# Kernel optimization log

Measured on AMD Instinct MI355X. Metric: run time of the kernel, lower is better.

## Reference

```python
import jax, jax.numpy as jnp
import numpy as np

SIGMA = 1.0  # init kwarg sigma

def _rbf_kernel(A):
    # K[i,j] = exp(-0.5 * ||a_i - a_j||^2 / sigma^2)
    sq = jnp.sum(A * A, axis=1)                      # [n]
    d2 = sq[:, None] + sq[None, :] - 2.0 * (A @ A.T)  # [n, n]
    return jnp.exp(-0.5 * d2 / (SIGMA ** 2))

def _double_center(K):
    # C K C with C = I - 11^T/n, done in O(n^2) via mean subtraction
    row = K.mean(axis=1, keepdims=True)
    col = K.mean(axis=0, keepdims=True)
    tot = K.mean()
    return K - row - col + tot

def setup_inputs() -> dict:
    key = jax.random.key(0)
    kx, ky = jax.random.split(key)
    X = jax.random.normal(kx, (4096, 512), dtype=jnp.float32)
    Y = jax.random.normal(ky, (4096, 512), dtype=jnp.float32)
    return {"X": X, "Y": Y}

def reference(X, Y):
    n = X.shape[0]
    KXc = _double_center(_rbf_kernel(X))
    KYc = _double_center(_rbf_kernel(Y))
    # trace(KX C KY C) = sum(center(KX) * center(KY)) since K symmetric, C idempotent
    hsic = jnp.sum(KXc * KYc) / ((n - 1) ** 2)
    return hsic
```

## Files before the change

kernel.cpp:

```cpp
#include <hip/hip_runtime.h>
#include <hip/hip_bf16.h>

namespace {

constexpr int N = 4096;
constexpr int D = 512;
constexpr int BM = 128;
constexpr int BK = 64;
constexpr int KITERS = D / BK;
constexpr int NB = N / BM;
constexpr int NBLK = NB * (NB + 1) / 2;
constexpr int TILEB = BM * BK;
constexpr int PANELB = BM * D;

constexpr size_t OFF_XB  = 0;
constexpr size_t OFF_YB  = (size_t)N * D;
constexpr size_t OFF_SQX = OFF_YB + (size_t)N * D;
constexpr size_t OFF_SQY = OFF_SQX + (size_t)N * 4;
constexpr size_t OFF_SX  = OFF_SQY + (size_t)N * 4;
constexpr size_t OFF_SY  = OFF_SX + (size_t)N * 4;
constexpr size_t OFF_T1  = OFF_SY + (size_t)N * 4;
constexpr size_t WS_NEED = OFF_T1 + 4;


constexpr float D2_SKIP = 240.f;

typedef __attribute__((ext_vector_type(4))) float floatx4;
typedef __attribute__((ext_vector_type(2))) long longx2;

__device__ inline void stage16(const void* g, void* l) {
  __builtin_amdgcn_global_load_lds(
      (const __attribute__((address_space(1))) unsigned int*)g,
      (__attribute__((address_space(3))) unsigned int*)l, 16, 0, 0);
}

__global__ void prep_kernel(const float* __restrict__ X, const float* __restrict__ Y,
                            unsigned char* __restrict__ Xf8, unsigned char* __restrict__ Yf8,
                            float* __restrict__ sqX, float* __restrict__ sqY,
                            float* __restrict__ sX, float* __restrict__ sY,
                            float* __restrict__ T1) {
  const int wave = threadIdx.x >> 6, lane = threadIdx.x & 63;
  const int row = blockIdx.x * 4 + wave;
  const int m = blockIdx.y;
  const float* __restrict__ src = m ? Y : X;
  unsigned char* __restrict__ dst = m ? Yf8 : Xf8;
  float* __restrict__ dsq = m ? sqY : sqX;

  if (threadIdx.x < 4) {
    float* z = m ? sY : sX;
    z[blockIdx.x * 4 + threadIdx.x] = 0.f;
  }
  if (blockIdx.x == 0 && m == 0 && threadIdx.x == 0) *T1 = 0.f;

  const float4* s4 = (const float4*)(src + (size_t)row * D);
  float4 v0 = s4[lane * 2];
  float4 v1 = s4[lane * 2 + 1];
  float acc = v0.x * v0.x + v0.y * v0.y + v0.z * v0.z + v0.w * v0.w
            + v1.x * v1.x + v1.y * v1.y + v1.z * v1.z + v1.w * v1.w;

  unsigned int w0 = 0, w1 = 0;
  w0 = __builtin_amdgcn_cvt_pk_fp8_f32(v0.x, v0.y, w0, false);
  w0 = __builtin_amdgcn_cvt_pk_fp8_f32(v0.z, v0.w, w0, true);
  w1 = __builtin_amdgcn_cvt_pk_fp8_f32(v1.x, v1.y, w1, false);
  w1 = __builtin_amdgcn_cvt_pk_fp8_f32(v1.z, v1.w, w1, true);
  const unsigned long long pk =
      (unsigned long long)w0 | ((unsigned long long)w1 << 32);

  const int p    = row >> 7;
  const int half = (row >> 6) & 1;
  const int nib  = (row >> 4) & 3;
  const int cl   = row & 15;
  const int ks   = lane >> 3;
  const int pass = (lane >> 2) & 1;
  const int quad = lane & 3;
  const size_t off = (size_t)p * PANELB + (size_t)ks * TILEB +
                     half * 4096 + nib * 1024 + quad * 256 + cl * 16 + pass * 8;
  *(unsigned long long*)(dst + off) = pk;

#pragma unroll
  for (int mm = 32; mm >= 1; mm >>= 1) acc += __shfl_xor(acc, mm, 64);
  if (lane == 0) dsq[row] = acc;
}

__launch_bounds__(256, 3)
__global__ void hsic_main(const unsigned char* __restrict__ Xf8,
                          const unsigned char* __restrict__ Yf8,
                          const float* __restrict__ sqX, const float* __restrict__ sqY,
                          float* __restrict__ sX, float* __restrict__ sY,
                          float* __restrict__ T1) {
  __shared__ __align__(16) unsigned char smem[2][2 * TILEB];

  const int b = blockIdx.x;
  int idx = (b & 7) * (NBLK / 8) + (b >> 3);

  const float nf = (float)NB + 0.5f;
  int bI = (int)(nf - sqrtf(nf * nf - 2.0f * (float)idx));
  if (bI < 0) bI = 0;
  if (bI >= NB) bI = NB - 1;
  while (bI * NB - bI * (bI - 1) / 2 > idx) --bI;
  while ((bI + 1) * NB - (bI + 1) * bI / 2 <= idx) ++bI;
  const int bJ = bI + (idx - (bI * NB - bI * (bI - 1) / 2));
  const bool offdiag = (bI != bJ);

  const int tid = threadIdx.x;
  const int lane = tid & 63, wave = tid >> 6;
  const int wm = wave >> 1, wn = wave & 1;
  const int quad = lane >> 4, cl = lane & 15;

  const unsigned char* gAx = Xf8 + (size_t)bI * PANELB;
  const unsigned char* gBx = Xf8 + (size_t)bJ * PANELB;
  const unsigned char* gAy = Yf8 + (size_t)bI * PANELB;
  const unsigned char* gBy = Yf8 + (size_t)bJ * PANELB;

  floatx4 accX[4][4];
  floatx4 accY[4][4];
#pragma unroll
  for (int i = 0; i < 4; ++i)
#pragma unroll
    for (int j = 0; j < 4; ++j) {
      accX[i][j] = (floatx4){0.f, 0.f, 0.f, 0.f};
      accY[i][j] = (floatx4){0.f, 0.f, 0.f, 0.f};
    }

  auto stage_all = [&](int iter, int buf) {
    const unsigned char* gA = (iter < KITERS) ? gAx : gAy;
    const unsigned char* gB = (iter < KITERS) ? gBx : gBy;
    const size_t ks0 = (size_t)(iter & (KITERS - 1)) * TILEB;
#pragma unroll
    for (int h = 0; h < 2; ++h) {
      const int c = tid + h * 256;
      const size_t goff = ks0 + (size_t)c * 16;
      stage16(gA + goff, &smem[buf][0 * TILEB + c * 16]);
      if (offdiag) stage16(gB + goff, &smem[buf][1 * TILEB + c * 16]);
    }
  };

  auto compute_tile = [&](const unsigned char* A, const unsigned char* B,
                          floatx4 (&acc)[4][4]) {
    longx2 bf[4];
#pragma unroll
    for (int ni = 0; ni < 4; ++ni)
      bf[ni] = *(const longx2*)&B[wn * 4096 + ni * 1024 + (lane << 4)];
#pragma unroll
    for (int mi = 0; mi < 4; ++mi) {
      const longx2 af = *(const longx2*)&A[wm * 4096 + mi * 1024 + (lane << 4)];
#pragma unroll
      for (int ni = 0; ni < 4; ++ni) {
        acc[mi][ni] = __builtin_amdgcn_mfma_f32_16x16x32_fp8_fp8(af[0], bf[ni][0], acc[mi][ni], 0, 0, 0);
        acc[mi][ni] = __builtin_amdgcn_mfma_f32_16x16x32_fp8_fp8(af[1], bf[ni][1], acc[mi][ni], 0, 0, 0);
      }
    }
  };

  stage_all(0, 0);

  for (int iter = 0; iter < 2 * KITERS; ++iter) {
    const int buf = iter & 1;
    __syncthreads();
    if (iter + 1 < 2 * KITERS) stage_all(iter + 1, buf ^ 1);

    const unsigned char* A = &smem[buf][0];
    const unsigned char* B = offdiag ? &smem[buf][TILEB] : &smem[buf][0];
    if (iter < KITERS) compute_tile(A, B, accX);
    else               compute_tile(A, B, accY);
  }

  const int Ib = bI * BM + wm * 64;
  const int Jb = bJ * BM + wn * 64;
  float t1l = 0.f;
  float rx[4][4], ry[4][4];
  float cx[4], cy[4];
#pragma unroll
  for (int mi = 0; mi < 4; ++mi)
#pragma unroll
    for (int r = 0; r < 4; ++r) { rx[mi][r] = 0.f; ry[mi][r] = 0.f; }
#pragma unroll
  for (int ni = 0; ni < 4; ++ni) { cx[ni] = 0.f; cy[ni] = 0.f; }

  bool wave_any = false;

#pragma unroll
  for (int mi = 0; mi < 4; ++mi) {
    const int ig0 = Ib + mi * 16 + quad * 4;
    float sxi[4], syi[4];
#pragma unroll
    for (int r = 0; r < 4; ++r) { sxi[r] = sqX[ig0 + r]; syi[r] = sqY[ig0 + r]; }
#pragma unroll
    for (int ni = 0; ni < 4; ++ni) {
      const int jg = Jb + ni * 16 + cl;
      const float sxj = sqX[jg];
      const float syj = sqY[jg];
      float d2x[4], d2y[4];
      bool lflag = false;
#pragma unroll
      for (int r = 0; r < 4; ++r) {
        const int ig = ig0 + r;
        d2x[r] = sxi[r] + sxj - 2.f * accX[mi][ni][r];
        d2y[r] = syi[r] + syj - 2.f * accY[mi][ni][r];
        lflag |= (d2x[r] < D2_SKIP) | (d2y[r] < D2_SKIP) | (ig == jg);
      }
      if (__any(lflag)) {
        wave_any = true;
#pragma unroll
        for (int r = 0; r < 4; ++r) {
          const int ig = ig0 + r;
          float kx, ky;
          if (ig == jg) {
            kx = 1.f; ky = 1.f;
          } else {
            kx = __expf(-0.5f * d2x[r]);
            ky = __expf(-0.5f * d2y[r]);
          }
          t1l += kx * ky;
          rx[mi][r] += kx;
          ry[mi][r] += ky;
          cx[ni] += kx;
          cy[ni] += ky;
        }
      }
    }
  }

  if (wave_any) {
#pragma unroll
    for (int mi = 0; mi < 4; ++mi)
#pragma unroll
      for (int r = 0; r < 4; ++r) {
        float vx = rx[mi][r], vy = ry[mi][r];
#pragma unroll
        for (int mm = 1; mm < 16; mm <<= 1) {
          vx += __shfl_xor(vx, mm, 16);
          vy += __shfl_xor(vy, mm, 16);
        }
        rx[mi][r] = vx; ry[mi][r] = vy;
      }
    if (cl == 0) {
#pragma unroll
      for (int mi = 0; mi < 4; ++mi)
#pragma unroll
        for (int r = 0; r < 4; ++r) {
          const int row = Ib + mi * 16 + quad * 4 + r;
          atomicAdd(&sX[row], rx[mi][r]);
          atomicAdd(&sY[row], ry[mi][r]);
        }
    }

    if (offdiag) {
#pragma unroll
      for (int ni = 0; ni < 4; ++ni) {
        float vx = cx[ni], vy = cy[ni];
        vx += __shfl_xor(vx, 16, 64); vy += __shfl_xor(vy, 16, 64);
        vx += __shfl_xor(vx, 32, 64); vy += __shfl_xor(vy, 32, 64);
        if (quad == 0) {
          const int col = Jb + ni * 16 + cl;
          atomicAdd(&sX[col], vx);
          atomicAdd(&sY[col], vy);
        }
      }
    }

    t1l *= offdiag ? 2.f : 1.f;
#pragma unroll
    for (int mm = 1; mm < 64; mm <<= 1) t1l += __shfl_xor(t1l, mm, 64);
  }
  __shared__ float tred[4];
  if (lane == 0) tred[wave] = t1l;
  __syncthreads();
  if (tid == 0) {
    const float t = tred[0] + tred[1] + tred[2] + tred[3];
    if (t != 0.f) atomicAdd(T1, t);
  }
}

__global__ void final_kernel(const float* __restrict__ sX, const float* __restrict__ sY,
                             const float* __restrict__ T1, float* __restrict__ out) {
  const int tid = threadIdx.x;
  float dp = 0.f, sa = 0.f, sb = 0.f;
  for (int i = tid; i < N; i += 256) {
    float a = sX[i], b = sY[i];
    dp += a * b; sa += a; sb += b;
  }
#pragma unroll
  for (int mm = 1; mm < 64; mm <<= 1) {
    dp += __shfl_xor(dp, mm, 64);
    sa += __shfl_xor(sa, mm, 64);
    sb += __shfl_xor(sb, mm, 64);
  }
  __shared__ float r0[4], r1[4], r2[4];
  if ((tid & 63) == 0) { int w = tid >> 6; r0[w] = dp; r1[w] = sa; r2[w] = sb; }
  __syncthreads();
  if (tid == 0) {
    dp = r0[0] + r0[1] + r0[2] + r0[3];
    sa = r1[0] + r1[1] + r1[2] + r1[3];
    sb = r2[0] + r2[1] + r2[2] + r2[3];
    const float n = (float)N;
    const float total = T1[0] - (2.f / n) * dp + (sa * sb) / (n * n);
    out[0] = total / ((n - 1.f) * (n - 1.f));
  }
}

}

extern "C" void kernel_launch(void* const* d_in, const int* in_sizes, int n_in,
                              void* d_out, int out_size, void* d_ws, size_t ws_size,
                              hipStream_t stream) {
  const float* X = (const float*)d_in[0];
  const float* Y = (const float*)d_in[1];
  char* ws = (char*)d_ws;
  if (ws_size < WS_NEED) return;

  unsigned char* Xf8 = (unsigned char*)(ws + OFF_XB);
  unsigned char* Yf8 = (unsigned char*)(ws + OFF_YB);
  float* sqX = (float*)(ws + OFF_SQX);
  float* sqY = (float*)(ws + OFF_SQY);
  float* sX  = (float*)(ws + OFF_SX);
  float* sY  = (float*)(ws + OFF_SY);
  float* T1  = (float*)(ws + OFF_T1);
  float* out = (float*)d_out;

  prep_kernel<<<dim3(N / 4, 2), 256, 0, stream>>>(X, Y, Xf8, Yf8, sqX, sqY, sX, sY, T1);
  hsic_main<<<NBLK, 256, 0, stream>>>(Xf8, Yf8, sqX, sqY, sX, sY, T1);
  final_kernel<<<1, 256, 0, stream>>>(sX, sY, T1, out);
}
```

Measured before the change: 97.22 us.

## Share one accumulator set across X and Y Gram passes, keeping X kernel as packed bf16

The main kernel now uses a single 4x4 block of MFMA accumulators instead of separate X and Y sets. The X-side RBF epilogue runs inside the k-loop right after the last X iteration: it computes the exp values, does the row and column atomics, packs the X kernel values into bf16 pairs and zeroes the accumulators for the Y pass. The Y epilogue then unpacks those values to form the cross term, with a per-tile mask marking which X sub-tiles were computed. This is meant to cut accumulator register pressure and raise occupancy, at the cost of bf16 rounding of the X kernel values in the HSIC sum.

Result: no change. 96.92 us (-0.3%).

```diff
diff --git a/kernel.cpp b/kernel.cpp
--- a/kernel.cpp
+++ b/kernel.cpp
@@ -32,6 +32,10 @@
   __builtin_amdgcn_global_load_lds(
       (const __attribute__((address_space(1))) unsigned int*)g,
       (__attribute__((address_space(3))) unsigned int*)l, 16, 0, 0);
+}
+
+__device__ inline unsigned short bf16bits(float f) {
+  return __builtin_bit_cast(unsigned short, __float2bfloat16(f));
 }
 
 __global__ void prep_kernel(const float* __restrict__ X, const float* __restrict__ Y,
@@ -112,15 +116,11 @@
   const unsigned char* gAy = Yf8 + (size_t)bI * PANELB;
   const unsigned char* gBy = Yf8 + (size_t)bJ * PANELB;
 
-  floatx4 accX[4][4];
-  floatx4 accY[4][4];
+  floatx4 acc[4][4];
 #pragma unroll
   for (int i = 0; i < 4; ++i)
 #pragma unroll
-    for (int j = 0; j < 4; ++j) {
-      accX[i][j] = (floatx4){0.f, 0.f, 0.f, 0.f};
-      accY[i][j] = (floatx4){0.f, 0.f, 0.f, 0.f};
-    }
+    for (int j = 0; j < 4; ++j) acc[i][j] = (floatx4){0.f, 0.f, 0.f, 0.f};
 
   auto stage_all = [&](int iter, int buf) {
     const unsigned char* gA = (iter < KITERS) ? gAx : gAy;
@@ -135,22 +135,12 @@
     }
   };
 
-  auto compute_tile = [&](const unsigned char* A, const unsigned char* B,
-                          floatx4 (&acc)[4][4]) {
-    longx2 bf[4];
-#pragma unroll
-    for (int ni = 0; ni < 4; ++ni)
-      bf[ni] = *(const longx2*)&B[wn * 4096 + ni * 1024 + (lane << 4)];
-#pragma unroll
-    for (int mi = 0; mi < 4; ++mi) {
-      const longx2 af = *(const longx2*)&A[wm * 4096 + mi * 1024 + (lane << 4)];
-#pragma unroll
-      for (int ni = 0; ni < 4; ++ni) {
-        acc[mi][ni] = __builtin_amdgcn_mfma_f32_16x16x32_fp8_fp8(af[0], bf[ni][0], acc[mi][ni], 0, 0, 0);
-        acc[mi][ni] = __builtin_amdgcn_mfma_f32_16x16x32_fp8_fp8(af[1], bf[ni][1], acc[mi][ni], 0, 0, 0);
-      }
-    }
-  };
+  const int Ib = bI * BM + wm * 64;
+  const int Jb = bJ * BM + wn * 64;
+
+  unsigned int kxp[4][4][2];
+  unsigned int fmask = 0;
+  float t1l = 0.f;
 
   stage_all(0, 0);
 
@@ -161,104 +151,177 @@
 
     const unsigned char* A = &smem[buf][0];
     const unsigned char* B = offdiag ? &smem[buf][TILEB] : &smem[buf][0];
-    if (iter < KITERS) compute_tile(A, B, accX);
-    else               compute_tile(A, B, accY);
-  }
-
-  const int Ib = bI * BM + wm * 64;
-  const int Jb = bJ * BM + wn * 64;
-  float t1l = 0.f;
-  float rx[4][4], ry[4][4];
-  float cx[4], cy[4];
-#pragma unroll
-  for (int mi = 0; mi < 4; ++mi)
-#pragma unroll
-    for (int r = 0; r < 4; ++r) { rx[mi][r] = 0.f; ry[mi][r] = 0.f; }
-#pragma unroll
-  for (int ni = 0; ni < 4; ++ni) { cx[ni] = 0.f; cy[ni] = 0.f; }
-
-  bool wave_any = false;
-
-#pragma unroll
-  for (int mi = 0; mi < 4; ++mi) {
-    const int ig0 = Ib + mi * 16 + quad * 4;
-    float sxi[4], syi[4];
-#pragma unroll
-    for (int r = 0; r < 4; ++r) { sxi[r] = sqX[ig0 + r]; syi[r] = sqY[ig0 + r]; }
-#pragma unroll
-    for (int ni = 0; ni < 4; ++ni) {
-      const int jg = Jb + ni * 16 + cl;
-      const float sxj = sqX[jg];
-      const float syj = sqY[jg];
-      float d2x[4], d2y[4];
-      bool lflag = false;
-#pragma unroll
-      for (int r = 0; r < 4; ++r) {
-        const int ig = ig0 + r;
-        d2x[r] = sxi[r] + sxj - 2.f * accX[mi][ni][r];
-        d2y[r] = syi[r] + syj - 2.f * accY[mi][ni][r];
-        lflag |= (d2x[r] < D2_SKIP) | (d2y[r] < D2_SKIP) | (ig == jg);
-      }
-      if (__any(lflag)) {
-        wave_any = true;
+
+    longx2 bf[4];
+#pragma unroll
+    for (int ni = 0; ni < 4; ++ni)
+      bf[ni] = *(const longx2*)&B[wn * 4096 + ni * 1024 + (lane << 4)];
+#pragma unroll
+    for (int mi = 0; mi < 4; ++mi) {
+      const longx2 af = *(const longx2*)&A[wm * 4096 + mi * 1024 + (lane << 4)];
+#pragma unroll
+      for (int ni = 0; ni < 4; ++ni) {
+        acc[mi][ni] = __builtin_amdgcn_mfma_f32_16x16x32_fp8_fp8(af[0], bf[ni][0], acc[mi][ni], 0, 0, 0);
+        acc[mi][ni] = __builtin_amdgcn_mfma_f32_16x16x32_fp8_fp8(af[1], bf[ni][1], acc[mi][ni], 0, 0, 0);
+      }
+    }
+
+    if (iter == KITERS - 1) {
+      float rx[4][4];
+      float cx[4];
+#pragma unroll
+      for (int mi = 0; mi < 4; ++mi)
+#pragma unroll
+        for (int r = 0; r < 4; ++r) rx[mi][r] = 0.f;
+#pragma unroll
+      for (int ni = 0; ni < 4; ++ni) cx[ni] = 0.f;
+
+#pragma unroll
+      for (int mi = 0; mi < 4; ++mi) {
+        const int ig0 = Ib + mi * 16 + quad * 4;
+        float sxi[4];
+#pragma unroll
+        for (int r = 0; r < 4; ++r) sxi[r] = sqX[ig0 + r];
+#pragma unroll
+        for (int ni = 0; ni < 4; ++ni) {
+          const int jg = Jb + ni * 16 + cl;
+          const float sxj = sqX[jg];
+          float d2x[4];
+          bool lflag = false;
+#pragma unroll
+          for (int r = 0; r < 4; ++r) {
+            const int ig = ig0 + r;
+            d2x[r] = sxi[r] + sxj - 2.f * acc[mi][ni][r];
+            lflag |= (d2x[r] < D2_SKIP) | (ig == jg);
+          }
+          float kxv[4] = {0.f, 0.f, 0.f, 0.f};
+          if (__any(lflag)) {
+            fmask |= (1u << (mi * 4 + ni));
+#pragma unroll
+            for (int r = 0; r < 4; ++r) {
+              const int ig = ig0 + r;
+              kxv[r] = (ig == jg) ? 1.f : __expf(-0.5f * d2x[r]);
+              rx[mi][r] += kxv[r];
+              cx[ni] += kxv[r];
+            }
+          }
+          kxp[mi][ni][0] = (unsigned)bf16bits(kxv[0]) | ((unsigned)bf16bits(kxv[1]) << 16);
+          kxp[mi][ni][1] = (unsigned)bf16bits(kxv[2]) | ((unsigned)bf16bits(kxv[3]) << 16);
+          acc[mi][ni] = (floatx4){0.f, 0.f, 0.f, 0.f};
+        }
+      }
+
+      if (fmask != 0) {
+#pragma unroll
+        for (int mi = 0; mi < 4; ++mi)
+#pragma unroll
+          for (int r = 0; r < 4; ++r) {
+            float vx = rx[mi][r];
+#pragma unroll
+            for (int mm = 1; mm < 16; mm <<= 1) vx += __shfl_xor(vx, mm, 16);
+            rx[mi][r] = vx;
+          }
+        if (cl == 0) {
+#pragma unroll
+          for (int mi = 0; mi < 4; ++mi)
+#pragma unroll
+            for (int r = 0; r < 4; ++r)
+              atomicAdd(&sX[Ib + mi * 16 + quad * 4 + r], rx[mi][r]);
+        }
+        if (offdiag) {
+#pragma unroll
+          for (int ni = 0; ni < 4; ++ni) {
+            float vx = cx[ni];
+            vx += __shfl_xor(vx, 16, 64);
+            vx += __shfl_xor(vx, 32, 64);
+            if (quad == 0) atomicAdd(&sX[Jb + ni * 16 + cl], vx);
+          }
+        }
+      }
+    }
+  }
+
+  {
+    float ry[4][4];
+    float cy[4];
+    bool anyy = false;
+#pragma unroll
+    for (int mi = 0; mi < 4; ++mi)
+#pragma unroll
+      for (int r = 0; r < 4; ++r) ry[mi][r] = 0.f;
+#pragma unroll
+    for (int ni = 0; ni < 4; ++ni) cy[ni] = 0.f;
+
+#pragma unroll
+    for (int mi = 0; mi < 4; ++mi) {
+      const int ig0 = Ib + mi * 16 + quad * 4;
+      float syi[4];
+#pragma unroll
+      for (int r = 0; r < 4; ++r) syi[r] = sqY[ig0 + r];
+#pragma unroll
+      for (int ni = 0; ni < 4; ++ni) {
+        const int jg = Jb + ni * 16 + cl;
+        const float syj = sqY[jg];
+        float d2y[4];
+        bool lflag = false;
 #pragma unroll
         for (int r = 0; r < 4; ++r) {
           const int ig = ig0 + r;
-          float kx, ky;
-          if (ig == jg) {
-            kx = 1.f; ky = 1.f;
-          } else {
-            kx = __expf(-0.5f * d2x[r]);
-            ky = __expf(-0.5f * d2y[r]);
-          }
-          t1l += kx * ky;
-          rx[mi][r] += kx;
-          ry[mi][r] += ky;
-          cx[ni] += kx;
-          cy[ni] += ky;
-        }
-      }
-    }
-  }
-
-  if (wave_any) {
-#pragma unroll
-    for (int mi = 0; mi < 4; ++mi)
-#pragma unroll
-      for (int r = 0; r < 4; ++r) {
-        float vx = rx[mi][r], vy = ry[mi][r];
-#pragma unroll
-        for (int mm = 1; mm < 16; mm <<= 1) {
-          vx += __shfl_xor(vx, mm, 16);
-          vy += __shfl_xor(vy, mm, 16);
-        }
-        rx[mi][r] = vx; ry[mi][r] = vy;
-      }
-    if (cl == 0) {
+          d2y[r] = syi[r] + syj - 2.f * acc[mi][ni][r];
+          lflag |= (d2y[r] < D2_SKIP) | (ig == jg);
+        }
+        const bool xb = (fmask >> (mi * 4 + ni)) & 1u;
+        if (__any(lflag) || xb) {
+          anyy = true;
+          float kyv[4];
+#pragma unroll
+          for (int r = 0; r < 4; ++r) {
+            const int ig = ig0 + r;
+            kyv[r] = (ig == jg) ? 1.f : __expf(-0.5f * d2y[r]);
+            ry[mi][r] += kyv[r];
+            cy[ni] += kyv[r];
+          }
+          if (xb) {
+            const float kx0 = __builtin_bit_cast(float, (kxp[mi][ni][0] & 0xFFFFu) << 16);
+            const float kx1 = __builtin_bit_cast(float, kxp[mi][ni][0] & 0xFFFF0000u);
+            const float kx2 = __builtin_bit_cast(float, (kxp[mi][ni][1] & 0xFFFFu) << 16);
+            const float kx3 = __builtin_bit_cast(float, kxp[mi][ni][1] & 0xFFFF0000u);
+            t1l += kx0 * kyv[0] + kx1 * kyv[1] + kx2 * kyv[2] + kx3 * kyv[3];
+          }
+        }
+      }
+    }
+
+    if (anyy) {
 #pragma unroll
       for (int mi = 0; mi < 4; ++mi)
 #pragma unroll
         for (int r = 0; r < 4; ++r) {
-          const int row = Ib + mi * 16 + quad * 4 + r;
-          atomicAdd(&sX[row], rx[mi][r]);
-          atomicAdd(&sY[row], ry[mi][r]);
-        }
-    }
-
-    if (offdiag) {
-#pragma unroll
-      for (int ni = 0; ni < 4; ++ni) {
-        float vx = cx[ni], vy = cy[ni];
-        vx += __shfl_xor(vx, 16, 64); vy += __shfl_xor(vy, 16, 64);
-        vx += __shfl_xor(vx, 32, 64); vy += __shfl_xor(vy, 32, 64);
-        if (quad == 0) {
-          const int col = Jb + ni * 16 + cl;
-          atomicAdd(&sX[col], vx);
-          atomicAdd(&sY[col], vy);
-        }
-      }
-    }
-
+          float vy = ry[mi][r];
+#pragma unroll
+          for (int mm = 1; mm < 16; mm <<= 1) vy += __shfl_xor(vy, mm, 16);
+          ry[mi][r] = vy;
+        }
+      if (cl == 0) {
+#pragma unroll
+        for (int mi = 0; mi < 4; ++mi)
+#pragma unroll
+          for (int r = 0; r < 4; ++r)
+            atomicAdd(&sY[Ib + mi * 16 + quad * 4 + r], ry[mi][r]);
+      }
+      if (offdiag) {
+#pragma unroll
+        for (int ni = 0; ni < 4; ++ni) {
+          float vy = cy[ni];
+          vy += __shfl_xor(vy, 16, 64);
+          vy += __shfl_xor(vy, 32, 64);
+          if (quad == 0) atomicAdd(&sY[Jb + ni * 16 + cl], vy);
+        }
+      }
+    }
+  }
+
+  if (fmask != 0) {
     t1l *= offdiag ? 2.f : 1.f;
 #pragma unroll
     for (int mm = 1; mm < 64; mm <<= 1) t1l += __shfl_xor(t1l, mm, 64);
```
